# Kernel optimization log

Measured on AMD Instinct MI355X. Metric: run time of the kernel, lower is better.

Reference implementation:

```python
import jax, jax.numpy as jnp
import numpy as np

NUM_EMBEDDINGS = 8192
EMBEDDING_DIM = 256
COMMITMENT_COST = 0.25


def setup_inputs() -> dict:
    key = jax.random.key(0)
    kz, kw = jax.random.split(key)
    z = jax.random.normal(kz, (65536, EMBEDDING_DIM), dtype=jnp.float32)
    # nn.Embedding init: uniform(-1/K, 1/K)
    W = jax.random.uniform(kw, (NUM_EMBEDDINGS, EMBEDDING_DIM), dtype=jnp.float32,
                           minval=-1.0 / NUM_EMBEDDINGS, maxval=1.0 / NUM_EMBEDDINGS)
    return {"z": z, "W": W}


def reference(z, W):
    # distances[n, k] = ||z_n||^2 + ||W_k||^2 - 2 z_n . W_k  -> [N, K]
    distances = (jnp.sum(z * z, axis=1, keepdims=True)
                 + jnp.sum(W * W, axis=1)
                 - 2.0 * jnp.matmul(z, W.T))
    encoding_indices = jnp.argmin(distances, axis=1)  # [N]
    # one-hot @ W is just a gather of codebook rows
    quantized = W[encoding_indices]  # [N, D]
    e_latent_loss = jnp.mean((jax.lax.stop_gradient(quantized) - z) ** 2)
    q_latent_loss = jnp.mean((quantized - jax.lax.stop_gradient(z)) ** 2)
    loss = q_latent_loss + COMMITMENT_COST * e_latent_loss
    # straight-through estimator
    quantized_st = z + jax.lax.stop_gradient(quantized - z)
    return quantized_st, loss, encoding_indices[:, None]
```

## Files before the change

### kernel.cpp

```cpp
#include <hip/hip_runtime.h>

#define N_ROWS 65536
#define K_CODES 8192
#define DIM 256
#define CAP 56

#define LOSS_OFF (N_ROWS * DIM)
#define IDX_OFF (LOSS_OFF + 1)
#define OUT_WBF_U16 0
#define OUT_ZBF_U16 2097152
#define OUT_CAND_F 9437184

#define WS_LOSS 0
#define WS_ZNORM 64
#define WS_WNORM (WS_ZNORM + N_ROWS)
#define WS_MARGIN (WS_WNORM + K_CODES)
#define WS_CUT0 (WS_MARGIN + N_ROWS)
#define WS_CNT (WS_CUT0 + N_ROWS)
#define WS_OVF (WS_CNT + N_ROWS)
#define WS_OVFLIST (WS_OVF + 1)
#define WS_SLOT (((WS_OVFLIST + N_ROWS) + 1) & ~1)

typedef __bf16 bf16x8 __attribute__((ext_vector_type(8)));
typedef float f32x4 __attribute__((ext_vector_type(4)));


__device__ __forceinline__ float mul_rn_nofma(float a, float b) {
  float r;
  asm("v_mul_f32 %0, %1, %2" : "=v"(r) : "v"(a), "v"(b));
  return r;
}

__device__ __forceinline__ unsigned int f2bf(float f) {
  unsigned int u = __float_as_uint(f);
  return (u + 0x7FFFu + ((u >> 16) & 1u)) >> 16;
}

__device__ float dot_chain(const float* __restrict__ zp, const float* __restrict__ wp) {
  float acc = 0.0f;
#pragma unroll 8
  for (int d4 = 0; d4 < 64; ++d4) {
    const float4 a = *(const float4*)(zp + d4 * 4);
    const float4 b = *(const float4*)(wp + d4 * 4);
    acc = fmaf(a.x, b.x, acc);
    acc = fmaf(a.y, b.y, acc);
    acc = fmaf(a.z, b.z, acc);
    acc = fmaf(a.w, b.w, acc);
  }
  return acc;
}

__device__ __forceinline__ void glds16(const void* g, void* l) {
  __builtin_amdgcn_global_load_lds(
      (const __attribute__((address_space(1))) void*)(unsigned long long)(size_t)g,
      (__attribute__((address_space(3))) void*)(unsigned int)(size_t)l, 16, 0, 0);
}


__global__ void prep_kernel(const float* __restrict__ z, const float* __restrict__ W,
                            float* __restrict__ ws, unsigned short* __restrict__ outu) {
  const int tid = threadIdx.x;
  const int l = tid & 63, w = tid >> 6;
  const int j = l & 7, b = (l >> 3) & 1, rw = l >> 4;
  const int row = blockIdx.x * 16 + w * 4 + rw;
  const bool isz = (row < N_ROWS);
  const float* src = isz ? (z + (size_t)row * DIM + b * 128)
                         : (W + (size_t)(row - N_ROWS) * DIM + b * 128);
  unsigned short* dst = isz ? (outu + OUT_ZBF_U16 + (size_t)row * DIM + b * 128)
                            : (outu + OUT_WBF_U16 + (size_t)(row - N_ROWS) * DIM + b * 128);
  float a0 = src[j];
  dst[j] = (unsigned short)f2bf(a0);
  float r = mul_rn_nofma(a0, a0);
  float s = fabsf(a0);
  for (int i = 8; i < 128; i += 8) {
    const float v = src[i + j];
    dst[i + j] = (unsigned short)f2bf(v);
    r = r + mul_rn_nofma(v, v);
    s = s + fabsf(v);
  }
  r = r + __shfl_xor(r, 1, 64);
  r = r + __shfl_xor(r, 2, 64);
  r = r + __shfl_xor(r, 4, 64);
  r = r + __shfl_xor(r, 8, 64);
  s = s + __shfl_xor(s, 1, 64);
  s = s + __shfl_xor(s, 2, 64);
  s = s + __shfl_xor(s, 4, 64);
  s = s + __shfl_xor(s, 8, 64);
  if ((l & 15) == 0) {
    if (isz) {
      ws[WS_ZNORM + row] = r;
      const float margin = 2.0e-6f * s + 4.0e-5f;
      ws[WS_MARGIN + row] = margin;
      ws[WS_CUT0 + row] = 3.10f * sqrtf(r) * 7.0467e-5f - margin;
      ((unsigned int*)ws)[WS_CNT + row] = 0u;
    } else {
      ws[WS_WNORM + (row - N_ROWS)] = r;
    }
  }
  if (blockIdx.x == 0 && tid == 0) {
    ws[WS_LOSS] = 0.0f;
    ((unsigned int*)ws)[WS_OVF] = 0u;
  }
}

__global__ __launch_bounds__(256) void gemm_screen_kernel(
    const unsigned short* __restrict__ zbf, const unsigned short* __restrict__ wbf,
    float* __restrict__ ws, uint2* __restrict__ candp) {
  __shared__ __align__(16) unsigned short As[2][128][32];
  __shared__ __align__(16) unsigned short Bs[2][128][32];
  __shared__ float cutbuf[128];

  const int tid = threadIdx.x;
  const int w = tid >> 6, l = tid & 63;
  const int lr = l & 15, lq = l >> 4;
  const int wr = (w >> 1) * 64, wc = (w & 1) * 64;
  const int rowBase = blockIdx.y * 128, colBase = blockIdx.x * 128;

  unsigned int* cntp = (unsigned int*)ws + WS_CNT;

  if (tid < 128) cutbuf[tid] = ws[WS_CUT0 + rowBase + tid];

  f32x4 acc[4][4];
#pragma unroll
  for (int mi = 0; mi < 4; ++mi)
#pragma unroll
    for (int ni = 0; ni < 4; ++ni) acc[mi][ni] = (f32x4){0.f, 0.f, 0.f, 0.f};

  const int ga = (l & 3) ^ ((l >> 3) & 3);
  auto STAGE = [&](int c, int b) {
#pragma unroll
    for (int j = 0; j < 2; ++j) {
      const int r_l = w * 32 + j * 16 + (l >> 2);
      glds16(zbf + (size_t)(rowBase + r_l) * DIM + c * 32 + ga * 8,
             &As[b][w * 32 + j * 16][0]);
      glds16(wbf + (size_t)(colBase + r_l) * DIM + c * 32 + ga * 8,
             &Bs[b][w * 32 + j * 16][0]);
    }
  };

  auto COMPUTE = [&](int b) {
    bf16x8 af[4], bfr[4];
    const int ch = (lq ^ ((lr >> 1) & 3)) * 8;
#pragma unroll
    for (int mi = 0; mi < 4; ++mi) af[mi] = *(const bf16x8*)&As[b][wr + mi * 16 + lr][ch];
#pragma unroll
    for (int ni = 0; ni < 4; ++ni) bfr[ni] = *(const bf16x8*)&Bs[b][wc + ni * 16 + lr][ch];
#pragma unroll
    for (int mi = 0; mi < 4; ++mi)
#pragma unroll
      for (int ni = 0; ni < 4; ++ni)
        acc[mi][ni] =
            __builtin_amdgcn_mfma_f32_16x16x32_bf16(af[mi], bfr[ni], acc[mi][ni], 0, 0, 0);
  };

  STAGE(0, 0);
  STAGE(1, 1);
#pragma unroll
  for (int c = 0; c < 8; ++c) {
    if (c < 7)
      asm volatile("s_waitcnt vmcnt(4)" ::: "memory");
    else
      asm volatile("s_waitcnt vmcnt(0)" ::: "memory");
    __builtin_amdgcn_sched_barrier(0);
    __builtin_amdgcn_s_barrier();
    __builtin_amdgcn_sched_barrier(0);
    COMPUTE(c & 1);
    __builtin_amdgcn_sched_barrier(0);
    __builtin_amdgcn_s_barrier();
    if (c < 6) STAGE(c + 2, c & 1);
  }

#pragma unroll
  for (int mi = 0; mi < 4; ++mi)
#pragma unroll
    for (int r = 0; r < 4; ++r) {
      const int lrow = wr + mi * 16 + lq * 4 + r;
      const float cut = cutbuf[lrow];
#pragma unroll
      for (int ni = 0; ni < 4; ++ni) {
        if (acc[mi][ni][r] >= cut) {
          const int grow = rowBase + lrow;
          const int gcol = colBase + wc + ni * 16 + lr;
          const unsigned int pos = atomicAdd(&cntp[grow], 1u);
          if (pos < CAP) {
            uint2 e;
            e.x = __float_as_uint(acc[mi][ni][r]);
            e.y = (unsigned int)gcol;
            candp[(size_t)grow * CAP + pos] = e;
          }
        }
      }
    }
}

__global__ void recheck_kernel(const float* __restrict__ z, const float* __restrict__ W,
                               float* __restrict__ ws, const uint2* __restrict__ candp,
                               float* __restrict__ out) {
  const int lane = threadIdx.x & 63;
  const int row = blockIdx.x * 4 + (threadIdx.x >> 6);
  const unsigned int cv = ((const unsigned int*)ws)[WS_CNT + row];
  const float margin = ws[WS_MARGIN + row];
  const float cut0 = ws[WS_CUT0 + row];
  bool fb = (cv == 0u) || (cv > CAP);
  uint2 e;
  e.x = 0u; e.y = 0u;
  float av = -3.4e38f;
  if (!fb && lane < (int)cv) {
    e = candp[(size_t)row * CAP + lane];
    av = __uint_as_float(e.x);
  }
  float candmax = av;
#pragma unroll
  for (int s = 1; s < 64; s <<= 1) candmax = fmaxf(candmax, __shfl_xor(candmax, s, 64));
  if (!fb && candmax - margin < cut0) fb = true;
  if (fb) {
    if (lane == 0) {
      ((unsigned long long*)((unsigned int*)ws + WS_SLOT))[row] = ~0ull;
      const unsigned int p = atomicAdd(&((unsigned int*)ws)[WS_OVF], 1u);
      ((unsigned int*)ws)[WS_OVFLIST + p] = (unsigned int)row;
      out[IDX_OFF + row] = -1.0f;
    }
    return;
  }
  const float fcut = candmax - margin;
  unsigned long long key = ~0ull;
  if (lane < (int)cv && av >= fcut) {
    const int k = (int)e.y;
    const float zn = ws[WS_ZNORM + row];
    const float m = dot_chain(z + (size_t)row * DIM, W + (size_t)k * DIM);
    const float dist = (zn + ws[WS_WNORM + k]) - 2.0f * m;
    key = ((unsigned long long)__float_as_uint(dist) << 32) | (unsigned int)k;
  }
#pragma unroll
  for (int s = 1; s < 64; s <<= 1) {
    const unsigned long long o = (unsigned long long)__shfl_xor((long long)key, s, 64);
    key = (o < key) ? o : key;
  }
  if (lane == 0) out[IDX_OFF + row] = (float)(unsigned int)(key & 0xffffffffull);
}

__global__ void fallback_compute(const float* __restrict__ z, const float* __restrict__ W,
                                 float* __restrict__ ws) {
  __shared__ unsigned long long part[4];
  const unsigned int n = ((const unsigned int*)ws)[WS_OVF];
  unsigned long long* slots = (unsigned long long*)((unsigned int*)ws + WS_SLOT);
  const unsigned int total = n * 32u;
  for (unsigned int item = blockIdx.x; item < total; item += gridDim.x) {
    const int row = (int)((const unsigned int*)ws)[WS_OVFLIST + (item >> 5)];
    const int k = (int)(item & 31u) * 256 + threadIdx.x;
    const float zn = ws[WS_ZNORM + row];
    const float m = dot_chain(z + (size_t)row * DIM, W + (size_t)k * DIM);
    const float dist = (zn + ws[WS_WNORM + k]) - 2.0f * m;
    unsigned long long key =
        ((unsigned long long)__float_as_uint(dist) << 32) | (unsigned int)k;
#pragma unroll
    for (int s = 1; s < 64; s <<= 1) {
      const unsigned long long o = __shfl_xor((long long)key, s, 64);
      key = (o < key) ? o : key;
    }
    if ((threadIdx.x & 63) == 0) part[threadIdx.x >> 6] = key;
    __syncthreads();
    if (threadIdx.x == 0) {
      unsigned long long b = part[0];
      b = (part[1] < b) ? part[1] : b;
      b = (part[2] < b) ? part[2] : b;
      b = (part[3] < b) ? part[3] : b;
      atomicMin(&slots[row], b);
    }
    __syncthreads();
  }
}

__global__ void gather_loss_kernel(const float* __restrict__ z, const float* __restrict__ W,
                                   float* __restrict__ out, float* __restrict__ ws) {
  const int tid = threadIdx.x;
  const int rowBase = blockIdx.x * 64;
  float lsum = 0.0f;
  for (int p = 0; p < 16; ++p) {
    const int row = rowBase + p * 4 + (tid >> 6);
    const int c4 = tid & 63;
    int idx = (int)out[IDX_OFF + row];
    if (idx < 0) {
      const unsigned long long key =
          ((const unsigned long long*)((const unsigned int*)ws + WS_SLOT))[row];
      idx = (int)(unsigned int)(key & 0xffffffffull);
      out[IDX_OFF + row] = (float)idx;
    }
    const float4 zv = *(const float4*)(z + (size_t)row * DIM + c4 * 4);
    const float4 qv = *(const float4*)(W + (size_t)idx * DIM + c4 * 4);
    float4 t, o;
    t.x = qv.x - zv.x; t.y = qv.y - zv.y; t.z = qv.z - zv.z; t.w = qv.w - zv.w;
    o.x = zv.x + t.x;  o.y = zv.y + t.y;  o.z = zv.z + t.z;  o.w = zv.w + t.w;
    *(float4*)(out + (size_t)row * DIM + c4 * 4) = o;
    lsum += t.x * t.x + t.y * t.y + t.z * t.z + t.w * t.w;
  }
#pragma unroll
  for (int m = 1; m < 64; m <<= 1) lsum += __shfl_xor(lsum, m, 64);
  __shared__ float part[4];
  if ((tid & 63) == 0) part[tid >> 6] = lsum;
  __syncthreads();
  if (tid == 0) atomicAdd(&ws[WS_LOSS], (part[0] + part[1]) + (part[2] + part[3]));
}

__global__ void finalize_kernel(const float* __restrict__ ws, float* __restrict__ out) {
  if (threadIdx.x == 0 && blockIdx.x == 0) {
    const float mean = ws[WS_LOSS] / (float)(N_ROWS * DIM);
    out[LOSS_OFF] = mean + 0.25f * mean;
  }
}

extern "C" void kernel_launch(void* const* d_in, const int* in_sizes, int n_in,
                              void* d_out, int out_size, void* d_ws, size_t ws_size,
                              hipStream_t stream) {
  (void)in_sizes; (void)n_in; (void)out_size; (void)ws_size;
  const float* z = (const float*)d_in[0];
  const float* W = (const float*)d_in[1];
  float* out = (float*)d_out;
  float* ws = (float*)d_ws;
  unsigned short* outu = (unsigned short*)d_out;
  const unsigned short* wbf = outu + OUT_WBF_U16;
  const unsigned short* zbf = outu + OUT_ZBF_U16;
  uint2* candp = (uint2*)((float*)d_out + OUT_CAND_F);

  hipLaunchKernelGGL(prep_kernel, dim3((N_ROWS + K_CODES) / 16), dim3(256), 0, stream,
                     z, W, ws, outu);
  hipLaunchKernelGGL(gemm_screen_kernel, dim3(K_CODES / 128, N_ROWS / 128), dim3(256),
                     0, stream, zbf, wbf, ws, candp);
  hipLaunchKernelGGL(recheck_kernel, dim3(N_ROWS / 4), dim3(256), 0, stream,
                     z, W, ws, candp, out);
  hipLaunchKernelGGL(fallback_compute, dim3(2048), dim3(256), 0, stream, z, W, ws);
  hipLaunchKernelGGL(gather_loss_kernel, dim3(N_ROWS / 64), dim3(256), 0, stream,
                     z, W, out, ws);
  hipLaunchKernelGGL(finalize_kernel, dim3(1), dim3(64), 0, stream, ws, out);
}
```

Measured before the change: 987.2 us.

## Make GEMM screen blocks persistent over eight row tiles per column tile

```diff
diff --git a/kernel.cpp b/kernel.cpp
--- a/kernel.cpp
+++ b/kernel.cpp
@@ -108,43 +108,43 @@
     float* __restrict__ ws, uint2* __restrict__ candp) {
   __shared__ __align__(16) unsigned short As[2][128][32];
   __shared__ __align__(16) unsigned short Bs[2][128][32];
-  __shared__ float cutbuf[128];
 
   const int tid = threadIdx.x;
   const int w = tid >> 6, l = tid & 63;
   const int lr = l & 15, lq = l >> 4;
   const int wr = (w >> 1) * 64, wc = (w & 1) * 64;
-  const int rowBase = blockIdx.y * 128, colBase = blockIdx.x * 128;
+  const int colBase = blockIdx.x * 128;
+  const int gBase = blockIdx.y * 1024;
 
   unsigned int* cntp = (unsigned int*)ws + WS_CNT;
 
-  if (tid < 128) cutbuf[tid] = ws[WS_CUT0 + rowBase + tid];
-
-  f32x4 acc[4][4];
-#pragma unroll
-  for (int mi = 0; mi < 4; ++mi)
-#pragma unroll
-    for (int ni = 0; ni < 4; ++ni) acc[mi][ni] = (f32x4){0.f, 0.f, 0.f, 0.f};
-
-  const int ga = (l & 3) ^ ((l >> 3) & 3);
-  auto STAGE = [&](int c, int b) {
+  const int ga0 = (l & 3) ^ ((l >> 3) & 3);
+  auto STAGE = [&](int u, int b) {
+    const int t = u >> 3, c = u & 7;
 #pragma unroll
     for (int j = 0; j < 2; ++j) {
       const int r_l = w * 32 + j * 16 + (l >> 2);
-      glds16(zbf + (size_t)(rowBase + r_l) * DIM + c * 32 + ga * 8,
+      glds16(zbf + (size_t)(gBase + t * 128 + r_l) * DIM + c * 32 + ga0 * 8,
              &As[b][w * 32 + j * 16][0]);
-      glds16(wbf + (size_t)(colBase + r_l) * DIM + c * 32 + ga * 8,
+      glds16(wbf + (size_t)(colBase + r_l) * DIM + c * 32 + ga0 * 8,
              &Bs[b][w * 32 + j * 16][0]);
     }
   };
+
+  f32x4 acc[4][4];
+#pragma unroll
+  for (int mi = 0; mi < 4; ++mi)
+#pragma unroll
+    for (int ni = 0; ni < 4; ++ni) acc[mi][ni] = (f32x4){0.f, 0.f, 0.f, 0.f};
+
+  const int chA = (lq ^ ((lr >> 1) & 3)) * 8;
 
   auto COMPUTE = [&](int b) {
     bf16x8 af[4], bfr[4];
-    const int ch = (lq ^ ((lr >> 1) & 3)) * 8;
-#pragma unroll
-    for (int mi = 0; mi < 4; ++mi) af[mi] = *(const bf16x8*)&As[b][wr + mi * 16 + lr][ch];
-#pragma unroll
-    for (int ni = 0; ni < 4; ++ni) bfr[ni] = *(const bf16x8*)&Bs[b][wc + ni * 16 + lr][ch];
+#pragma unroll
+    for (int mi = 0; mi < 4; ++mi) af[mi] = *(const bf16x8*)&As[b][wr + mi * 16 + lr][chA];
+#pragma unroll
+    for (int ni = 0; ni < 4; ++ni) bfr[ni] = *(const bf16x8*)&Bs[b][wc + ni * 16 + lr][chA];
 #pragma unroll
     for (int mi = 0; mi < 4; ++mi)
 #pragma unroll
@@ -155,42 +155,52 @@
 
   STAGE(0, 0);
   STAGE(1, 1);
-#pragma unroll
-  for (int c = 0; c < 8; ++c) {
-    if (c < 7)
+  for (int u = 0; u < 64; ++u) {
+    if (u < 63)
       asm volatile("s_waitcnt vmcnt(4)" ::: "memory");
     else
       asm volatile("s_waitcnt vmcnt(0)" ::: "memory");
     __builtin_amdgcn_sched_barrier(0);
     __builtin_amdgcn_s_barrier();
     __builtin_amdgcn_sched_barrier(0);
-    COMPUTE(c & 1);
+    COMPUTE(u & 1);
     __builtin_amdgcn_sched_barrier(0);
     __builtin_amdgcn_s_barrier();
-    if (c < 6) STAGE(c + 2, c & 1);
-  }
-
-#pragma unroll
-  for (int mi = 0; mi < 4; ++mi)
-#pragma unroll
-    for (int r = 0; r < 4; ++r) {
-      const int lrow = wr + mi * 16 + lq * 4 + r;
-      const float cut = cutbuf[lrow];
-#pragma unroll
-      for (int ni = 0; ni < 4; ++ni) {
-        if (acc[mi][ni][r] >= cut) {
-          const int grow = rowBase + lrow;
-          const int gcol = colBase + wc + ni * 16 + lr;
-          const unsigned int pos = atomicAdd(&cntp[grow], 1u);
-          if (pos < CAP) {
-            uint2 e;
-            e.x = __float_as_uint(acc[mi][ni][r]);
-            e.y = (unsigned int)gcol;
-            candp[(size_t)grow * CAP + pos] = e;
+    if (u < 62) STAGE(u + 2, u & 1);
+
+    if ((u & 7) == 7) {
+      const int rowBase = gBase + (u >> 3) * 128;
+#pragma unroll
+      for (int mi = 0; mi < 4; ++mi) {
+        const float4 cutv =
+            *(const float4*)(ws + WS_CUT0 + rowBase + wr + mi * 16 + lq * 4);
+        const float cuta[4] = {cutv.x, cutv.y, cutv.z, cutv.w};
+#pragma unroll
+        for (int r = 0; r < 4; ++r) {
+          const int lrow = wr + mi * 16 + lq * 4 + r;
+          const float cut = cuta[r];
+#pragma unroll
+          for (int ni = 0; ni < 4; ++ni) {
+            if (acc[mi][ni][r] >= cut) {
+              const int grow = rowBase + lrow;
+              const int gcol = colBase + wc + ni * 16 + lr;
+              const unsigned int pos = atomicAdd(&cntp[grow], 1u);
+              if (pos < CAP) {
+                uint2 e;
+                e.x = __float_as_uint(acc[mi][ni][r]);
+                e.y = (unsigned int)gcol;
+                candp[(size_t)grow * CAP + pos] = e;
+              }
+            }
           }
         }
+        acc[mi][0] = (f32x4){0.f, 0.f, 0.f, 0.f};
+        acc[mi][1] = (f32x4){0.f, 0.f, 0.f, 0.f};
+        acc[mi][2] = (f32x4){0.f, 0.f, 0.f, 0.f};
+        acc[mi][3] = (f32x4){0.f, 0.f, 0.f, 0.f};
       }
     }
+  }
 }
 
 __global__ void recheck_kernel(const float* __restrict__ z, const float* __restrict__ W,
@@ -324,7 +334,7 @@
 
   hipLaunchKernelGGL(prep_kernel, dim3((N_ROWS + K_CODES) / 16), dim3(256), 0, stream,
                      z, W, ws, outu);
-  hipLaunchKernelGGL(gemm_screen_kernel, dim3(K_CODES / 128, N_ROWS / 128), dim3(256),
+  hipLaunchKernelGGL(gemm_screen_kernel, dim3(K_CODES / 128, N_ROWS / 1024), dim3(256),
                      0, stream, zbf, wbf, ws, candp);
   hipLaunchKernelGGL(recheck_kernel, dim3(N_ROWS / 4), dim3(256), 0, stream,
                      z, W, ws, candp, out);
```

Result: slower. 1.353 ms (+37.0%).
